# Kernel optimization log

Hardware: AMD Instinct MI355X
Metric: run time of the kernel (lower is better)

Reference implementation:

```python
import jax, jax.numpy as jnp
import numpy as np
from jax import lax

R = 2  # upscale factor


def setup_inputs() -> dict:
    key = jax.random.key(0)
    k1, k2, k3 = jax.random.split(key, 3)
    x = jax.random.normal(k1, (16, 192, 192, 64), dtype=jnp.float32)
    # Conv2D kernel: HWIO, filters = r*r*64 = 256
    W = jax.random.normal(k2, (3, 3, 64, 256), dtype=jnp.float32) * 0.05
    b = jax.random.normal(k3, (256,), dtype=jnp.float32) * 0.05
    return {"x": x, "W": W, "b": b}


def reference(x, W, b):
    # Conv2D, stride 1, 'same' padding, NHWC/HWIO
    y = lax.conv_general_dilated(
        x, W, window_strides=(1, 1), padding="SAME",
        dimension_numbers=("NHWC", "HWIO", "NHWC")) + b
    # phase_shift: O[B, i*r+q, j*r+p, k] = y[B, i, j, k*r*r + p*r + q]
    B, a, bdim, c = y.shape
    cp = c // (R * R)
    y = y.reshape(B, a, bdim, cp, R, R)          # [B,a,b,k,p,q]
    y = jnp.transpose(y, (0, 1, 5, 2, 4, 3))     # [B,a,q,b,p,k]
    return y.reshape(B, a * R, bdim * R, cp)
```

## Files before the change

kernel.cpp:

```cpp
#include <hip/hip_runtime.h>
#include <stdint.h>

typedef short bf16x8 __attribute__((ext_vector_type(8)));
typedef float f32x4  __attribute__((ext_vector_type(4)));

#define GLOAD_LDS16(gp, lp) \
    __builtin_amdgcn_global_load_lds((const __attribute__((address_space(1))) void*)(gp), \
                                     (__attribute__((address_space(3))) void*)(lp), 16, 0, 0)

__device__ __forceinline__ uint32_t bfbits(float f) {
    uint32_t u = __builtin_bit_cast(uint32_t, f);
    u += 0x7FFFu + ((u >> 16) & 1u);
    return u >> 16;
}
__device__ __forceinline__ uint32_t pk2(float a, float b) {
    return bfbits(a) | (bfbits(b) << 16);
}

__global__ void xcvt_kernel(const float* __restrict__ x, short* __restrict__ xb) {
    const int total = 16 * 194 * 194 * 8;
    for (int i = blockIdx.x * 256 + threadIdx.x; i < total; i += gridDim.x * 256) {
        int g  = i & 7;
        int t  = i >> 3;
        int wp = t % 194; t /= 194;
        int hp = t % 194;
        int nn = t / 194;
        uint4 r = {0u, 0u, 0u, 0u};
        if (hp >= 1 && hp <= 192 && wp >= 1 && wp <= 192) {
            const float* s = x + (((size_t)nn * 192 + (hp - 1)) * 192 + (wp - 1)) * 64 + g * 8;
            f32x4 a = *(const f32x4*)s;
            f32x4 b = *(const f32x4*)(s + 4);
            r.x = pk2(a[0], a[1]); r.y = pk2(a[2], a[3]);
            r.z = pk2(b[0], b[1]); r.w = pk2(b[2], b[3]);
        }
        *(uint4*)(xb + (size_t)i * 8) = r;
    }
}

__global__ void wt_kernel(const float* __restrict__ W, short* __restrict__ Wt) {
    int idx = blockIdx.x * 256 + threadIdx.x;
    if (idx >= 147456) return;
    int t  = idx >> 14;
    int r  = idx & 16383;
    int c  = r >> 12;
    int j  = (r >> 6) & 63;
    int ic = r & 63;
    Wt[idx] = (short)bfbits(W[(t * 64 + ic) * 256 + j * 4 + c]);
}

#define NT 6
#define A_SLOT 4224
#define A_SH   (10 * A_SLOT)
#define B_SH   (9 * 64 * 64)

__global__ __launch_bounds__(512, 2) void conv_ps_kernel(
    const short* __restrict__ xb, const short* __restrict__ Wt,
    const float* __restrict__ bias, float* __restrict__ out)
{
    __shared__ short smem[ (A_SH + B_SH) ];
    short* As = smem;
    short* Bs = smem + A_SH;

    const int tid   = threadIdx.x;
    const int lane  = tid & 63;
    const int wv    = tid >> 6;
    const int row_l = lane & 15;
    const int grp   = lane >> 4;
    const int b7    = row_l & 7;

    const int raw = blockIdx.x;
    const int lb  = (raw & 7) * 96 + (raw >> 3);
    const int c   = lb & 3;
    const int wt  = (lb >> 2) % 3;
    const int hg  = (lb / 12) & 3;
    const int n   = lb / 48;
    const int w0  = wt * 64;
    const int hbase = hg * 48;
    const int q = c & 1, p = (c >> 1) & 1;

    {
        const short* wsrc = Wt + c * 4096;
        for (int k = wv; k < 72; k += 8) {
            int t   = k >> 3, j8 = k & 7;
            int cch = j8 * 64 + lane;
            int j   = cch >> 3, s1 = cch & 7;
            int ss  = s1 ^ (j & 7);
            GLOAD_LDS16(wsrc + t * 16384 + j * 64 + ss * 8,
                        (char*)Bs + t * 8192 + j8 * 1024);
        }
    }
    for (int k = wv; k < 90; k += 8) {
        int rl  = k / 9, jj = k % 9;
        int row = hbase - 1 + rl;
        int slot = (row + 1) % 10;
        int cch = jj * 64 + lane;
        int wpos = cch >> 3, g1 = cch & 7;
        int gs   = g1 ^ (wpos & 7);
        const short* src = xb + (((size_t)n * 194 + (row + 1)) * 194 + (w0 + wpos)) * 64 + gs * 8;
        void* dst = (char*)As + slot * 8448 + jj * 1024;
        if (jj < 8)            GLOAD_LDS16(src, dst);
        else if (lane < 16)    GLOAD_LDS16(src, dst);
    }
    __syncthreads();

    float bv[4];
    #pragma unroll
    for (int nt = 0; nt < 4; ++nt)
        bv[nt] = bias[(nt * 16 + row_l) * 4 + c];

    #pragma unroll 1
    for (int it = 0; it < NT; ++it) {
        const int h0 = hbase + it * 8;

        f32x4 acc[4][4];
        #pragma unroll
        for (int i = 0; i < 4; ++i)
            #pragma unroll
            for (int j = 0; j < 4; ++j)
                acc[i][j] = (f32x4){bv[j], bv[j], bv[j], bv[j]};

        int sl[3];
        #pragma unroll
        for (int dy = 0; dy < 3; ++dy) sl[dy] = (h0 + wv + dy) % 10;

        #pragma unroll
        for (int dy = 0; dy < 3; ++dy) {
            #pragma unroll
            for (int dx = 0; dx < 3; ++dx) {
                const int t  = dy * 3 + dx;
                const int rd = row_l + dx;
                const int a7 = rd & 7;
                const int aB = sl[dy] * A_SLOT + rd * 64;
                const int bB = t * 4096 + row_l * 64;
                #pragma unroll
                for (int ks = 0; ks < 2; ++ks) {
                    const int kg = ks * 4 + grp;
                    const short* ap = &As[aB + ((kg ^ a7) << 3)];
                    const short* bp = &Bs[bB + ((kg ^ b7) << 3)];
                    bf16x8 af[4], bfr[4];
                    #pragma unroll
                    for (int mt = 0; mt < 4; ++mt) af[mt]  = *(const bf16x8*)(ap + mt * 1024);
                    #pragma unroll
                    for (int nt = 0; nt < 4; ++nt) bfr[nt] = *(const bf16x8*)(bp + nt * 1024);
                    #pragma unroll
                    for (int mt = 0; mt < 4; ++mt)
                        #pragma unroll
                        for (int nt = 0; nt < 4; ++nt)
                            acc[mt][nt] = __builtin_amdgcn_mfma_f32_16x16x32_bf16(
                                af[mt], bfr[nt], acc[mt][nt], 0, 0, 0);
                }
            }
        }

        const int h = h0 + wv;
        const long rowb = ((long)(n * 384 + 2 * h + q)) * 384;

        if (it < NT - 1) {
            asm volatile("s_waitcnt lgkmcnt(0)" ::: "memory");
            __builtin_amdgcn_sched_barrier(0);
            __builtin_amdgcn_s_barrier();
            __builtin_amdgcn_sched_barrier(0);

            for (int k = wv; k < 72; k += 8) {
                int rl  = k / 9, jj = k % 9;
                int row = h0 + 9 + rl;
                int slot = (row + 1) % 10;
                int cch = jj * 64 + lane;
                int wpos = cch >> 3, g1 = cch & 7;
                int gs   = g1 ^ (wpos & 7);
                const short* src = xb + (((size_t)n * 194 + (row + 1)) * 194 + (w0 + wpos)) * 64 + gs * 8;
                void* dst = (char*)As + slot * 8448 + jj * 1024;
                if (jj < 8)         GLOAD_LDS16(src, dst);
                else if (lane < 16) GLOAD_LDS16(src, dst);
            }
            asm volatile("" ::: "memory");
            __builtin_amdgcn_sched_barrier(0);

            #pragma unroll
            for (int mt = 0; mt < 4; ++mt) {
                float* po = out + ((rowb + 2 * (w0 + mt * 16 + grp * 4) + p) * 64 + row_l);
                #pragma unroll
                for (int nt = 0; nt < 4; ++nt)
                    #pragma unroll
                    for (int jv = 0; jv < 4; ++jv)
                        po[jv * 128 + nt * 16] = acc[mt][nt][jv];
            }

            asm volatile("s_waitcnt vmcnt(63)" ::: "memory");
            __builtin_amdgcn_sched_barrier(0);
            __builtin_amdgcn_s_barrier();
            __builtin_amdgcn_sched_barrier(0);
        } else {
            #pragma unroll
            for (int mt = 0; mt < 4; ++mt) {
                float* po = out + ((rowb + 2 * (w0 + mt * 16 + grp * 4) + p) * 64 + row_l);
                #pragma unroll
                for (int nt = 0; nt < 4; ++nt)
                    #pragma unroll
                    for (int jv = 0; jv < 4; ++jv)
                        po[jv * 128 + nt * 16] = acc[mt][nt][jv];
            }
        }
    }
}

extern "C" void kernel_launch(void* const* d_in, const int* in_sizes, int n_in,
                              void* d_out, int out_size, void* d_ws, size_t ws_size,
                              hipStream_t stream) {
    const float* x = (const float*)d_in[0];
    const float* W = (const float*)d_in[1];
    const float* b = (const float*)d_in[2];
    float* out = (float*)d_out;

    const size_t xb_bytes = (size_t)16 * 194 * 194 * 64 * 2;
    short* xbuf = (short*)d_ws;
    short* Wt   = (short*)((char*)d_ws + xb_bytes);

    hipLaunchKernelGGL(xcvt_kernel, dim3(2048), dim3(256), 0, stream, x, xbuf);
    hipLaunchKernelGGL(wt_kernel, dim3(576), dim3(256), 0, stream, W, Wt);
    hipLaunchKernelGGL(conv_ps_kernel, dim3(768), dim3(512), 0, stream, xbuf, Wt, b, out);
}
```

Before: 277.8 us.

## Stream conv weights from global into registers and widen LDS input ring

Weights are no longer staged in LDS. Each wave now loads them straight from global memory into registers, double-buffered one tap ahead of the MFMAs. The freed LDS is used to grow the input-row ring from 10 to 18 slots. That lets the next 8 rows be prefetched at the start of each iteration without the pre-prefetch barrier. The trade-off is repeated global/L1 weight traffic per wave, and in-order vmcnt waits that may tie weight-load latency to the outstanding prefetch and stores.

```diff
diff --git a/kernel.cpp b/kernel.cpp
--- a/kernel.cpp
+++ b/kernel.cpp
@@ -49,24 +49,21 @@
 }
 
 #define NT 6
+#define RING 18
 #define A_SLOT 4224
-#define A_SH   (10 * A_SLOT)
-#define B_SH   (9 * 64 * 64)
+#define A_SH   (RING * A_SLOT)
 
 __global__ __launch_bounds__(512, 2) void conv_ps_kernel(
     const short* __restrict__ xb, const short* __restrict__ Wt,
     const float* __restrict__ bias, float* __restrict__ out)
 {
-    __shared__ short smem[ (A_SH + B_SH) ];
-    short* As = smem;
-    short* Bs = smem + A_SH;
+    __shared__ short As[A_SH];
 
     const int tid   = threadIdx.x;
     const int lane  = tid & 63;
     const int wv    = tid >> 6;
     const int row_l = lane & 15;
     const int grp   = lane >> 4;
-    const int b7    = row_l & 7;
 
     const int raw = blockIdx.x;
     const int lb  = (raw & 7) * 96 + (raw >> 3);
@@ -78,21 +75,12 @@
     const int hbase = hg * 48;
     const int q = c & 1, p = (c >> 1) & 1;
 
-    {
-        const short* wsrc = Wt + c * 4096;
-        for (int k = wv; k < 72; k += 8) {
-            int t   = k >> 3, j8 = k & 7;
-            int cch = j8 * 64 + lane;
-            int j   = cch >> 3, s1 = cch & 7;
-            int ss  = s1 ^ (j & 7);
-            GLOAD_LDS16(wsrc + t * 16384 + j * 64 + ss * 8,
-                        (char*)Bs + t * 8192 + j8 * 1024);
-        }
-    }
+    const short* wsrc = Wt + c * 4096;
+
     for (int k = wv; k < 90; k += 8) {
         int rl  = k / 9, jj = k % 9;
         int row = hbase - 1 + rl;
-        int slot = (row + 1) % 10;
+        int slot = (row + 1) % RING;
         int cch = jj * 64 + lane;
         int wpos = cch >> 3, g1 = cch & 7;
         int gs   = g1 ^ (wpos & 7);
@@ -108,63 +96,43 @@
     for (int nt = 0; nt < 4; ++nt)
         bv[nt] = bias[(nt * 16 + row_l) * 4 + c];
 
+    bf16x8 bA[2][4], bB[2][4];
+
+#define LOADB(DST, T) do { \
+    _Pragma("unroll") for (int ks = 0; ks < 2; ++ks) \
+        _Pragma("unroll") for (int nt_ = 0; nt_ < 4; ++nt_) \
+            DST[ks][nt_] = *(const bf16x8*)(wsrc + (T) * 16384 + \
+                             (nt_ * 16 + row_l) * 64 + (ks * 4 + grp) * 8); \
+} while (0)
+
+#define TAP(T, CUR, NXT, LOADNEXT) do { \
+    const int dy_ = (T) / 3, dx_ = (T) % 3; \
+    const int rd_ = row_l + dx_; \
+    const int a7_ = rd_ & 7; \
+    const int aB_ = sl[dy_] * A_SLOT + rd_ * 64; \
+    bf16x8 af[2][4]; \
+    _Pragma("unroll") for (int ks = 0; ks < 2; ++ks) { \
+        const short* ap = &As[aB_ + (((ks * 4 + grp) ^ a7_) << 3)]; \
+        _Pragma("unroll") for (int mt_ = 0; mt_ < 4; ++mt_) \
+            af[ks][mt_] = *(const bf16x8*)(ap + mt_ * 1024); \
+    } \
+    if (LOADNEXT) LOADB(NXT, (T) + 1); \
+    _Pragma("unroll") for (int ks = 0; ks < 2; ++ks) \
+        _Pragma("unroll") for (int mt_ = 0; mt_ < 4; ++mt_) \
+            _Pragma("unroll") for (int nt_ = 0; nt_ < 4; ++nt_) \
+                acc[mt_][nt_] = __builtin_amdgcn_mfma_f32_16x16x32_bf16( \
+                    af[ks][mt_], CUR[ks][nt_], acc[mt_][nt_], 0, 0, 0); \
+} while (0)
+
     #pragma unroll 1
     for (int it = 0; it < NT; ++it) {
         const int h0 = hbase + it * 8;
 
-        f32x4 acc[4][4];
-        #pragma unroll
-        for (int i = 0; i < 4; ++i)
-            #pragma unroll
-            for (int j = 0; j < 4; ++j)
-                acc[i][j] = (f32x4){bv[j], bv[j], bv[j], bv[j]};
-
-        int sl[3];
-        #pragma unroll
-        for (int dy = 0; dy < 3; ++dy) sl[dy] = (h0 + wv + dy) % 10;
-
-        #pragma unroll
-        for (int dy = 0; dy < 3; ++dy) {
-            #pragma unroll
-            for (int dx = 0; dx < 3; ++dx) {
-                const int t  = dy * 3 + dx;
-                const int rd = row_l + dx;
-                const int a7 = rd & 7;
-                const int aB = sl[dy] * A_SLOT + rd * 64;
-                const int bB = t * 4096 + row_l * 64;
-                #pragma unroll
-                for (int ks = 0; ks < 2; ++ks) {
-                    const int kg = ks * 4 + grp;
-                    const short* ap = &As[aB + ((kg ^ a7) << 3)];
-                    const short* bp = &Bs[bB + ((kg ^ b7) << 3)];
-                    bf16x8 af[4], bfr[4];
-                    #pragma unroll
-                    for (int mt = 0; mt < 4; ++mt) af[mt]  = *(const bf16x8*)(ap + mt * 1024);
-                    #pragma unroll
-                    for (int nt = 0; nt < 4; ++nt) bfr[nt] = *(const bf16x8*)(bp + nt * 1024);
-                    #pragma unroll
-                    for (int mt = 0; mt < 4; ++mt)
-                        #pragma unroll
-                        for (int nt = 0; nt < 4; ++nt)
-                            acc[mt][nt] = __builtin_amdgcn_mfma_f32_16x16x32_bf16(
-                                af[mt], bfr[nt], acc[mt][nt], 0, 0, 0);
-                }
-            }
-        }
-
-        const int h = h0 + wv;
-        const long rowb = ((long)(n * 384 + 2 * h + q)) * 384;
-
         if (it < NT - 1) {
-            asm volatile("s_waitcnt lgkmcnt(0)" ::: "memory");
-            __builtin_amdgcn_sched_barrier(0);
-            __builtin_amdgcn_s_barrier();
-            __builtin_amdgcn_sched_barrier(0);
-
             for (int k = wv; k < 72; k += 8) {
                 int rl  = k / 9, jj = k % 9;
                 int row = h0 + 9 + rl;
-                int slot = (row + 1) % 10;
+                int slot = (row + 1) % RING;
                 int cch = jj * 64 + lane;
                 int wpos = cch >> 3, g1 = cch & 7;
                 int gs   = g1 ^ (wpos & 7);
@@ -173,9 +141,34 @@
                 if (jj < 8)         GLOAD_LDS16(src, dst);
                 else if (lane < 16) GLOAD_LDS16(src, dst);
             }
-            asm volatile("" ::: "memory");
-            __builtin_amdgcn_sched_barrier(0);
-
+        }
+
+        LOADB(bA, 0);
+
+        f32x4 acc[4][4];
+        #pragma unroll
+        for (int i = 0; i < 4; ++i)
+            #pragma unroll
+            for (int j = 0; j < 4; ++j)
+                acc[i][j] = (f32x4){bv[j], bv[j], bv[j], bv[j]};
+
+        int sl[3];
+        #pragma unroll
+        for (int dy = 0; dy < 3; ++dy) sl[dy] = (h0 + wv + dy) % RING;
+
+        TAP(0, bA, bB, 1);
+        TAP(1, bB, bA, 1);
+        TAP(2, bA, bB, 1);
+        TAP(3, bB, bA, 1);
+        TAP(4, bA, bB, 1);
+        TAP(5, bB, bA, 1);
+        TAP(6, bA, bB, 1);
+        TAP(7, bB, bA, 1);
+        TAP(8, bA, bB, 0);
+
+        {
+            const int h = h0 + wv;
+            const long rowb = ((long)(n * 384 + 2 * h + q)) * 384;
             #pragma unroll
             for (int mt = 0; mt < 4; ++mt) {
                 float* po = out + ((rowb + 2 * (w0 + mt * 16 + grp * 4) + p) * 64 + row_l);
@@ -185,23 +178,17 @@
                     for (int jv = 0; jv < 4; ++jv)
                         po[jv * 128 + nt * 16] = acc[mt][nt][jv];
             }
-
+        }
+
+        if (it < NT - 1) {
             asm volatile("s_waitcnt vmcnt(63)" ::: "memory");
             __builtin_amdgcn_sched_barrier(0);
             __builtin_amdgcn_s_barrier();
             __builtin_amdgcn_sched_barrier(0);
-        } else {
-            #pragma unroll
-            for (int mt = 0; mt < 4; ++mt) {
-                float* po = out + ((rowb + 2 * (w0 + mt * 16 + grp * 4) + p) * 64 + row_l);
-                #pragma unroll
-                for (int nt = 0; nt < 4; ++nt)
-                    #pragma unroll
-                    for (int jv = 0; jv < 4; ++jv)
-                        po[jv * 128 + nt * 16] = acc[mt][nt][jv];
-            }
         }
     }
+#undef TAP
+#undef LOADB
 }
 
 extern "C" void kernel_launch(void* const* d_in, const int* in_sizes, int n_in,
```

Measured after the change: 515.4 us. 1.86x slower.
